# Optimization experiments

Measured on AMD Instinct MI355X. Metric: run time of the kernel, lower is better.

The kernel has to match this reference:

```python
import jax, jax.numpy as jnp
import numpy as np

B, S, D, H = 512, 64, 1024, 16  # seq_len=64 fixed by Reshape([-1,8,8,d_model])
DH = D // H


def setup_inputs() -> dict:
    key = jax.random.key(0)
    ks = jax.random.split(key, 5)
    w_scale = 0.02  # keep pre-softmax logits / activations in a sane range
    return {
        "x": jax.random.normal(ks[0], (B, S, D), jnp.float32),
        "wq_w": jax.random.normal(ks[1], (D, D), jnp.float32) * w_scale,
        "wq_b": jnp.zeros((D,), jnp.float32),
        "wk_w": jax.random.normal(ks[2], (D, D), jnp.float32) * w_scale,
        "wk_b": jnp.zeros((D,), jnp.float32),
        "wv_w": jax.random.normal(ks[3], (D, D), jnp.float32) * w_scale,
        "wv_b": jnp.zeros((D,), jnp.float32),
        "wo_w": jax.random.normal(ks[4], (D, D), jnp.float32) * w_scale,
        "wo_b": jnp.zeros((D,), jnp.float32),
    }


def _split_heads(t):
    # [B, S, D] -> [B, H, S, DH]
    b, s, _ = t.shape
    return t.reshape(b, s, H, DH).transpose(0, 2, 1, 3)


def reference(x, wq_w, wq_b, wk_w, wk_b, wv_w, wv_b, wo_w, wo_b):
    b, s, d = x.shape
    q = _split_heads(x @ wq_w + wq_b)
    k = _split_heads(x @ wk_w + wk_b)
    v = _split_heads(x @ wv_w + wv_b)
    # NOTE: original scales by sqrt(d_model), not sqrt(depth)
    scores = jnp.einsum("bhqd,bhkd->bhqk", q, k) / jnp.sqrt(jnp.float32(d))
    # original 'padding mask': (scores == 0) * 1e-9 added to scores
    scores = scores + (scores == 0).astype(scores.dtype) * 1e-9
    attn = jax.nn.softmax(scores, axis=-1)
    ctx = jnp.einsum("bhqk,bhkd->bhqd", attn, v)  # [B, H, S, DH]
    ctx = ctx.transpose(0, 2, 1, 3).reshape(b, s, d)  # [B, S, D]
    # keras Dense(..., activation='gelu') uses exact (erf) gelu by default
    out = jax.nn.gelu(ctx @ wo_w + wo_b, approximate=False)
    # Reshape([-1, 8, 8, D]) then squeeze -> [B, 8, 8, D]
    return out.reshape(b, 8, 8, d)
```

## Files before the change

### kernel.cpp

```cpp
#include <hip/hip_runtime.h>
#include <cstdint>
#include <math.h>

typedef float f32x4 __attribute__((ext_vector_type(4)));
typedef __bf16 bf16x8 __attribute__((ext_vector_type(8)));
typedef unsigned short u16x8 __attribute__((ext_vector_type(8)));
typedef unsigned short u16x4 __attribute__((ext_vector_type(4)));

typedef __attribute__((address_space(1))) const void* gas_cvptr;
typedef __attribute__((address_space(3))) void* las_vptr;

__device__ __forceinline__ unsigned short f32_to_bf16(float f) {
  uint32_t u = __builtin_bit_cast(uint32_t, f);
  u += 0x7FFFu + ((u >> 16) & 1u);
  return (unsigned short)(u >> 16);
}

__device__ __forceinline__ bf16x8 ld_bf16x8(const unsigned short* p) {
  return __builtin_bit_cast(bf16x8, *(const u16x8*)p);
}

__global__ void cvt_x(const float* __restrict__ x, unsigned short* __restrict__ xb, int n4) {
  int stride = gridDim.x * blockDim.x;
  for (int i = blockIdx.x * blockDim.x + threadIdx.x; i < n4; i += stride) {
    float4 v = ((const float4*)x)[i];
    u16x4 o = { f32_to_bf16(v.x), f32_to_bf16(v.y), f32_to_bf16(v.z), f32_to_bf16(v.w) };
    ((u16x4*)xb)[i] = o;
  }
}

__global__ void cvt_w(const float* __restrict__ wq, const float* __restrict__ wk,
                      const float* __restrict__ wv, const float* __restrict__ wo,
                      unsigned short* __restrict__ wqkvT, unsigned short* __restrict__ woT) {
  const int z = blockIdx.z;
  const float* __restrict__ w = (z == 0) ? wq : (z == 1) ? wk : (z == 2) ? wv : wo;
  unsigned short* __restrict__ out = (z < 3) ? (wqkvT + (size_t)z * 1024 * 1024) : woT;
  __shared__ float tile[64][65];
  const int r0 = blockIdx.y * 64;
  const int c0 = blockIdx.x * 64;
  const int t = threadIdx.x;
#pragma unroll
  for (int i = 0; i < 4; i++) {
    int row = (t >> 4) + i * 16;
    int col = (t & 15) * 4;
    float4 v = *(const float4*)&w[(size_t)(r0 + row) * 1024 + c0 + col];
    tile[row][col] = v.x; tile[row][col + 1] = v.y;
    tile[row][col + 2] = v.z; tile[row][col + 3] = v.w;
  }
  __syncthreads();
#pragma unroll
  for (int i = 0; i < 2; i++) {
    int nr = (t >> 3) + i * 32;
    int kc = (t & 7) * 8;
    u16x8 o;
#pragma unroll
    for (int j = 0; j < 8; j++) o[j] = f32_to_bf16(tile[kc + j][nr]);
    *(u16x8*)&out[(size_t)(c0 + nr) * 1024 + r0 + kc] = o;
  }
}

template <int EPI>
__global__ __launch_bounds__(256) void gemm_bt(
    const unsigned short* __restrict__ A, const unsigned short* __restrict__ Bt,
    const float* __restrict__ b0, const float* __restrict__ b1, const float* __restrict__ b2,
    unsigned short* __restrict__ Qb, unsigned short* __restrict__ Kb, unsigned short* __restrict__ Vb,
    float* __restrict__ Out, int Ncols, int Ktot) {
  __shared__ __align__(16) unsigned short As[128 * 32];
  __shared__ __align__(16) unsigned short Bs[128 * 32];
  const int nb = Ncols >> 7;
  const int tm = blockIdx.x / nb, tn = blockIdx.x % nb;
  const int rowBase = tm << 7, colBase = tn << 7;
  const int t = threadIdx.x;
  const int lane = t & 63, w = t >> 6;
  const int li = lane & 15, lg = lane >> 4;
  const int wr = (w >> 1) * 64, wc = (w & 1) * 64;

  f32x4 acc[4][4] = {};

  for (int kt = 0; kt < Ktot; kt += 32) {
    __syncthreads();
#pragma unroll
    for (int half = 0; half < 2; half++) {
      const int c = t + half * 256;
      const unsigned short* gA = A + (size_t)(rowBase + (c >> 2)) * Ktot + kt + (c & 3) * 8;
      __builtin_amdgcn_global_load_lds((gas_cvptr)gA,
          (las_vptr)(As + (size_t)(w * 64 + half * 256) * 8), 16, 0, 0);
      const unsigned short* gB = Bt + (size_t)(colBase + (c >> 2)) * Ktot + kt + (c & 3) * 8;
      __builtin_amdgcn_global_load_lds((gas_cvptr)gB,
          (las_vptr)(Bs + (size_t)(w * 64 + half * 256) * 8), 16, 0, 0);
    }
    __syncthreads();
    bf16x8 af[4], bfr[4];
#pragma unroll
    for (int m = 0; m < 4; m++) af[m] = ld_bf16x8(As + (wr + m * 16 + li) * 32 + lg * 8);
#pragma unroll
    for (int n = 0; n < 4; n++) bfr[n] = ld_bf16x8(Bs + (wc + n * 16 + li) * 32 + lg * 8);
#pragma unroll
    for (int m = 0; m < 4; m++)
#pragma unroll
      for (int n = 0; n < 4; n++)
        acc[m][n] = __builtin_amdgcn_mfma_f32_16x16x32_bf16(af[m], bfr[n], acc[m][n], 0, 0, 0);
  }

  if (EPI == 0) {
    const int part = colBase >> 10;
    const float* __restrict__ bias = (part == 0) ? b0 : (part == 1) ? b1 : b2;
    unsigned short* __restrict__ dst = (part == 0) ? Qb : (part == 1) ? Kb : Vb;
#pragma unroll
    for (int m = 0; m < 4; m++) {
      const int rowb = rowBase + wr + m * 16 + lg * 4;
#pragma unroll
      for (int r = 0; r < 4; r++) {
        const int row = rowb + r;
        const int b = row >> 6, s = row & 63;
#pragma unroll
        for (int n = 0; n < 4; n++) {
          const int col = colBase + wc + n * 16 + li;
          const int within = col & 1023;
          const int h = within >> 6, dh = within & 63;
          float v = acc[m][n][r] + bias[within];
          dst[(size_t)((b * 16 + h) * 64 + s) * 64 + dh] = f32_to_bf16(v);
        }
      }
    }
  } else {
#pragma unroll
    for (int m = 0; m < 4; m++) {
      const int rowb = rowBase + wr + m * 16 + lg * 4;
#pragma unroll
      for (int r = 0; r < 4; r++) {
#pragma unroll
        for (int n = 0; n < 4; n++) {
          const int col = colBase + wc + n * 16 + li;
          float v = acc[m][n][r] + b0[col];
          v = 0.5f * v * (1.0f + erff(v * 0.70710678118654752f));
          Out[(size_t)(rowb + r) * 1024 + col] = v;
        }
      }
    }
  }
}

__global__ __launch_bounds__(256) void attn(
    const unsigned short* __restrict__ Qb, const unsigned short* __restrict__ Kb,
    const unsigned short* __restrict__ Vb, unsigned short* __restrict__ ctx) {
  __shared__ __align__(16) unsigned short Qs[64][72];
  __shared__ __align__(16) unsigned short Ks[64][72];
  __shared__ __align__(16) unsigned short Vt[64][72];
  __shared__ __align__(16) unsigned short Ps[64][72];
  const int bh = blockIdx.x;
  const int b = bh >> 4, h = bh & 15;
  const int t = threadIdx.x, lane = t & 63, w = t >> 6;
  const int li = lane & 15, lg = lane >> 4;
  const unsigned short* __restrict__ Qg = Qb + (size_t)bh * 4096;
  const unsigned short* __restrict__ Kg = Kb + (size_t)bh * 4096;
  const unsigned short* __restrict__ Vg = Vb + (size_t)bh * 4096;

#pragma unroll
  for (int i = 0; i < 2; i++) {
    const int c = t + i * 256;
    const int row = c >> 3, col8 = (c & 7) * 8;
    *(u16x8*)&Qs[row][col8] = *(const u16x8*)&Qg[row * 64 + col8];
    *(u16x8*)&Ks[row][col8] = *(const u16x8*)&Kg[row * 64 + col8];
    u16x8 v = *(const u16x8*)&Vg[row * 64 + col8];
#pragma unroll
    for (int j = 0; j < 8; j++) Vt[col8 + j][row] = v[j];
  }
  __syncthreads();

  f32x4 sc[4] = {};
#pragma unroll
  for (int ks = 0; ks < 2; ks++) {
    bf16x8 qa = ld_bf16x8(&Qs[w * 16 + li][ks * 32 + lg * 8]);
#pragma unroll
    for (int n = 0; n < 4; n++) {
      bf16x8 kf = ld_bf16x8(&Ks[n * 16 + li][ks * 32 + lg * 8]);
      sc[n] = __builtin_amdgcn_mfma_f32_16x16x32_bf16(qa, kf, sc[n], 0, 0, 0);
    }
  }

#pragma unroll
  for (int r = 0; r < 4; r++) {
    float v0 = sc[0][r] * 0.03125f, v1 = sc[1][r] * 0.03125f;
    float v2 = sc[2][r] * 0.03125f, v3 = sc[3][r] * 0.03125f;
    float mx = fmaxf(fmaxf(v0, v1), fmaxf(v2, v3));
#pragma unroll
    for (int off = 1; off < 16; off <<= 1) mx = fmaxf(mx, __shfl_xor(mx, off, 64));
    float e0 = __expf(v0 - mx), e1 = __expf(v1 - mx);
    float e2 = __expf(v2 - mx), e3 = __expf(v3 - mx);
    float sum = e0 + e1 + e2 + e3;
#pragma unroll
    for (int off = 1; off < 16; off <<= 1) sum += __shfl_xor(sum, off, 64);
    float is = 1.0f / sum;
    const int q = w * 16 + lg * 4 + r;
    Ps[q][0 * 16 + li] = f32_to_bf16(e0 * is);
    Ps[q][1 * 16 + li] = f32_to_bf16(e1 * is);
    Ps[q][2 * 16 + li] = f32_to_bf16(e2 * is);
    Ps[q][3 * 16 + li] = f32_to_bf16(e3 * is);
  }
  __syncthreads();

  f32x4 oc[4] = {};
#pragma unroll
  for (int ks = 0; ks < 2; ks++) {
    bf16x8 pa = ld_bf16x8(&Ps[w * 16 + li][ks * 32 + lg * 8]);
#pragma unroll
    for (int n = 0; n < 4; n++) {
      bf16x8 vf = ld_bf16x8(&Vt[n * 16 + li][ks * 32 + lg * 8]);
      oc[n] = __builtin_amdgcn_mfma_f32_16x16x32_bf16(pa, vf, oc[n], 0, 0, 0);
    }
  }
#pragma unroll
  for (int n = 0; n < 4; n++)
#pragma unroll
    for (int r = 0; r < 4; r++)
      ctx[(size_t)(b * 64 + w * 16 + lg * 4 + r) * 1024 + h * 64 + n * 16 + li] =
          f32_to_bf16(oc[n][r]);
}

extern "C" void kernel_launch(void* const* d_in, const int* in_sizes, int n_in,
                              void* d_out, int out_size, void* d_ws, size_t ws_size,
                              hipStream_t stream) {
  const float* x  = (const float*)d_in[0];
  const float* wq = (const float*)d_in[1];
  const float* bq = (const float*)d_in[2];
  const float* wk = (const float*)d_in[3];
  const float* bk = (const float*)d_in[4];
  const float* wv = (const float*)d_in[5];
  const float* bv = (const float*)d_in[6];
  const float* wo = (const float*)d_in[7];
  const float* bo = (const float*)d_in[8];
  float* out = (float*)d_out;

  const int D = 1024;
  const int M = in_sizes[0] / D;

  char* ws = (char*)d_ws;
  unsigned short* xb    = (unsigned short*)ws;
  unsigned short* wqkvT = (unsigned short*)(ws + (size_t)M * 1024 * 2);
  unsigned short* woT   = wqkvT + (size_t)3 * 1024 * 1024;
  unsigned short* Qb    = woT + (size_t)1024 * 1024;
  unsigned short* Kb    = Qb + (size_t)M * 1024;
  unsigned short* Vb    = Kb + (size_t)M * 1024;
  unsigned short* ctx   = xb;

  cvt_x<<<2048, 256, 0, stream>>>(x, xb, M * D / 4);
  cvt_w<<<dim3(16, 16, 4), 256, 0, stream>>>(wq, wk, wv, wo, wqkvT, woT);
  gemm_bt<0><<<(M / 128) * (3072 / 128), 256, 0, stream>>>(
      xb, wqkvT, bq, bk, bv, Qb, Kb, Vb, nullptr, 3072, 1024);
  attn<<<(M / 64) * 16, 256, 0, stream>>>(Qb, Kb, Vb, ctx);
  gemm_bt<1><<<(M / 128) * (1024 / 128), 256, 0, stream>>>(
      ctx, woT, bo, nullptr, nullptr, nullptr, nullptr, nullptr, out, 1024, 1024);
}
```

Measured before the change: 490.7 us.

## Replace GEMM with 256x256 tile, 4-stage async LDS pipeline and XCD swizzle

Rewrites the projection GEMM kernel to use 256x256 output tiles with 512 threads, a 4-deep ring of LDS buffers filled by global_load_lds, and explicit vmcnt waits and barriers. This overlaps global loads with MFMA work across k-tiles and raises data reuse per block. It also remaps block ids so consecutive tiles land on the same XCD, and uses setprio around the MFMA bursts. The trade-offs are higher LDS use (128KB per block) and register pressure from 32 accumulators, plus fewer blocks for the output GEMM.

Result: faster. 428.5 us (-12.7%).

```diff
diff --git a/kernel.cpp b/kernel.cpp
--- a/kernel.cpp
+++ b/kernel.cpp
@@ -9,6 +9,12 @@
 
 typedef __attribute__((address_space(1))) const void* gas_cvptr;
 typedef __attribute__((address_space(3))) void* las_vptr;
+
+#define WAITV8 asm volatile("s_waitcnt vmcnt(8)" ::: "memory")
+#define WAITV4 asm volatile("s_waitcnt vmcnt(4)" ::: "memory")
+#define WAITV0 asm volatile("s_waitcnt vmcnt(0)" ::: "memory")
+#define WAITL0 asm volatile("s_waitcnt lgkmcnt(0)" ::: "memory")
+#define BAR()  __builtin_amdgcn_s_barrier()
 
 __device__ __forceinline__ unsigned short f32_to_bf16(float f) {
   uint32_t u = __builtin_bit_cast(uint32_t, f);
@@ -60,79 +66,127 @@
 }
 
 template <int EPI>
-__global__ __launch_bounds__(256) void gemm_bt(
+__global__ __launch_bounds__(512, 2) void gemm256(
     const unsigned short* __restrict__ A, const unsigned short* __restrict__ Bt,
     const float* __restrict__ b0, const float* __restrict__ b1, const float* __restrict__ b2,
     unsigned short* __restrict__ Qb, unsigned short* __restrict__ Kb, unsigned short* __restrict__ Vb,
-    float* __restrict__ Out, int Ncols, int Ktot) {
-  __shared__ __align__(16) unsigned short As[128 * 32];
-  __shared__ __align__(16) unsigned short Bs[128 * 32];
-  const int nb = Ncols >> 7;
-  const int tm = blockIdx.x / nb, tn = blockIdx.x % nb;
-  const int rowBase = tm << 7, colBase = tn << 7;
+    float* __restrict__ Out, int Ncols, int K) {
+  __shared__ __align__(16) unsigned short As[4][256][32];
+  __shared__ __align__(16) unsigned short Bs[4][256][32];
+  const int NT = K >> 5;
+  const int nb = Ncols >> 8;
+  const int nwg = gridDim.x;
+  const int cpx = nwg >> 3;
+  const int bid = blockIdx.x;
+  const int wg = (bid & 7) * cpx + (bid >> 3);
+  const int tm = wg / nb, tn = wg % nb;
+  const int rowBase = tm << 8, colBase = tn << 8;
   const int t = threadIdx.x;
-  const int lane = t & 63, w = t >> 6;
+  const int lane = t & 63;
+  const int w = t >> 6;
   const int li = lane & 15, lg = lane >> 4;
-  const int wr = (w >> 1) * 64, wc = (w & 1) * 64;
-
-  f32x4 acc[4][4] = {};
-
-  for (int kt = 0; kt < Ktot; kt += 32) {
-    __syncthreads();
-#pragma unroll
-    for (int half = 0; half < 2; half++) {
-      const int c = t + half * 256;
-      const unsigned short* gA = A + (size_t)(rowBase + (c >> 2)) * Ktot + kt + (c & 3) * 8;
-      __builtin_amdgcn_global_load_lds((gas_cvptr)gA,
-          (las_vptr)(As + (size_t)(w * 64 + half * 256) * 8), 16, 0, 0);
-      const unsigned short* gB = Bt + (size_t)(colBase + (c >> 2)) * Ktot + kt + (c & 3) * 8;
-      __builtin_amdgcn_global_load_lds((gas_cvptr)gB,
-          (las_vptr)(Bs + (size_t)(w * 64 + half * 256) * 8), 16, 0, 0);
-    }
-    __syncthreads();
-    bf16x8 af[4], bfr[4];
-#pragma unroll
-    for (int m = 0; m < 4; m++) af[m] = ld_bf16x8(As + (wr + m * 16 + li) * 32 + lg * 8);
-#pragma unroll
-    for (int n = 0; n < 4; n++) bfr[n] = ld_bf16x8(Bs + (wc + n * 16 + li) * 32 + lg * 8);
+  const int wm = w >> 2, wn = w & 3;
+  const int aRow0 = wm * 128;
+  const int bRow0 = wn * 64;
+
+  const int c0 = t, c1 = t + 512;
+  const int r0s = c0 >> 2, s0s = c0 & 3;
+  const int r1s = c1 >> 2, s1s = c1 & 3;
+  const unsigned short* gA0 = A + (size_t)(rowBase + r0s) * K + s0s * 8;
+  const unsigned short* gA1 = A + (size_t)(rowBase + r1s) * K + s1s * 8;
+  const unsigned short* gB0 = Bt + (size_t)(colBase + r0s) * K + s0s * 8;
+  const unsigned short* gB1 = Bt + (size_t)(colBase + r1s) * K + s1s * 8;
+
+#define STAGE_A(tile_) do { int b_ = (tile_) & 3; int kt_ = (tile_) << 5;                     \
+    __builtin_amdgcn_global_load_lds((gas_cvptr)(gA0 + kt_),                                  \
+        (las_vptr)(&As[b_][0][0] + c0 * 8), 16, 0, 0);                                        \
+    __builtin_amdgcn_global_load_lds((gas_cvptr)(gA1 + kt_),                                  \
+        (las_vptr)(&As[b_][0][0] + c1 * 8), 16, 0, 0); } while (0)
+#define STAGE_B(tile_) do { int b_ = (tile_) & 3; int kt_ = (tile_) << 5;                     \
+    __builtin_amdgcn_global_load_lds((gas_cvptr)(gB0 + kt_),                                  \
+        (las_vptr)(&Bs[b_][0][0] + c0 * 8), 16, 0, 0);                                        \
+    __builtin_amdgcn_global_load_lds((gas_cvptr)(gB1 + kt_),                                  \
+        (las_vptr)(&Bs[b_][0][0] + c1 * 8), 16, 0, 0); } while (0)
+
+  STAGE_A(0); STAGE_B(0);
+  STAGE_A(1); STAGE_B(1);
+  STAGE_A(2); STAGE_B(2);
+  WAITV8;
+  BAR();
+
+  f32x4 acc[8][4] = {};
+  bf16x8 af[4], bfr[4];
+
+  for (int tt = 0; tt < NT; ++tt) {
+    const unsigned short* ab = &As[tt & 3][0][0];
+    const unsigned short* bb = &Bs[tt & 3][0][0];
+#pragma unroll
+    for (int m = 0; m < 4; m++) af[m] = ld_bf16x8(ab + (aRow0 + m * 16 + li) * 32 + lg * 8);
+#pragma unroll
+    for (int n = 0; n < 4; n++) bfr[n] = ld_bf16x8(bb + (bRow0 + n * 16 + li) * 32 + lg * 8);
+    if (tt + 3 < NT) STAGE_A(tt + 3);
+    BAR();
+    WAITL0;
+    __builtin_amdgcn_s_setprio(1);
 #pragma unroll
     for (int m = 0; m < 4; m++)
 #pragma unroll
       for (int n = 0; n < 4; n++)
         acc[m][n] = __builtin_amdgcn_mfma_f32_16x16x32_bf16(af[m], bfr[n], acc[m][n], 0, 0, 0);
-  }
+    __builtin_amdgcn_s_setprio(0);
+    BAR();
+#pragma unroll
+    for (int m = 0; m < 4; m++)
+      af[m] = ld_bf16x8(ab + (aRow0 + 64 + m * 16 + li) * 32 + lg * 8);
+    if (tt + 3 < NT) STAGE_B(tt + 3);
+    BAR();
+    WAITL0;
+    __builtin_amdgcn_s_setprio(1);
+#pragma unroll
+    for (int m = 0; m < 4; m++)
+#pragma unroll
+      for (int n = 0; n < 4; n++)
+        acc[4 + m][n] = __builtin_amdgcn_mfma_f32_16x16x32_bf16(af[m], bfr[n], acc[4 + m][n], 0, 0, 0);
+    __builtin_amdgcn_s_setprio(0);
+    if (tt <= NT - 4)      WAITV8;
+    else if (tt == NT - 3) WAITV4;
+    else                   WAITV0;
+    BAR();
+  }
+#undef STAGE_A
+#undef STAGE_B
 
   if (EPI == 0) {
     const int part = colBase >> 10;
     const float* __restrict__ bias = (part == 0) ? b0 : (part == 1) ? b1 : b2;
     unsigned short* __restrict__ dst = (part == 0) ? Qb : (part == 1) ? Kb : Vb;
 #pragma unroll
-    for (int m = 0; m < 4; m++) {
-      const int rowb = rowBase + wr + m * 16 + lg * 4;
+    for (int mi = 0; mi < 8; mi++) {
+      const int rowb = rowBase + aRow0 + mi * 16 + lg * 4;
 #pragma unroll
       for (int r = 0; r < 4; r++) {
         const int row = rowb + r;
         const int b = row >> 6, s = row & 63;
 #pragma unroll
         for (int n = 0; n < 4; n++) {
-          const int col = colBase + wc + n * 16 + li;
+          const int col = colBase + bRow0 + n * 16 + li;
           const int within = col & 1023;
           const int h = within >> 6, dh = within & 63;
-          float v = acc[m][n][r] + bias[within];
+          float v = acc[mi][n][r] + bias[within];
           dst[(size_t)((b * 16 + h) * 64 + s) * 64 + dh] = f32_to_bf16(v);
         }
       }
     }
   } else {
 #pragma unroll
-    for (int m = 0; m < 4; m++) {
-      const int rowb = rowBase + wr + m * 16 + lg * 4;
+    for (int mi = 0; mi < 8; mi++) {
+      const int rowb = rowBase + aRow0 + mi * 16 + lg * 4;
 #pragma unroll
       for (int r = 0; r < 4; r++) {
 #pragma unroll
         for (int n = 0; n < 4; n++) {
-          const int col = colBase + wc + n * 16 + li;
-          float v = acc[m][n][r] + b0[col];
+          const int col = colBase + bRow0 + n * 16 + li;
+          float v = acc[mi][n][r] + b0[col];
           v = 0.5f * v * (1.0f + erff(v * 0.70710678118654752f));
           Out[(size_t)(rowb + r) * 1024 + col] = v;
         }
@@ -246,9 +300,9 @@
 
   cvt_x<<<2048, 256, 0, stream>>>(x, xb, M * D / 4);
   cvt_w<<<dim3(16, 16, 4), 256, 0, stream>>>(wq, wk, wv, wo, wqkvT, woT);
-  gemm_bt<0><<<(M / 128) * (3072 / 128), 256, 0, stream>>>(
+  gemm256<0><<<(M / 256) * (3072 / 256), 512, 0, stream>>>(
       xb, wqkvT, bq, bk, bv, Qb, Kb, Vb, nullptr, 3072, 1024);
   attn<<<(M / 64) * 16, 256, 0, stream>>>(Qb, Kb, Vb, ctx);
-  gemm_bt<1><<<(M / 128) * (1024 / 128), 256, 0, stream>>>(
+  gemm256<1><<<(M / 256) * (1024 / 256), 512, 0, stream>>>(
       ctx, woT, bo, nullptr, nullptr, nullptr, nullptr, nullptr, out, 1024, 1024);
 }
```
